# Optimization experiments

Hardware: AMD Instinct MI355X
Metric: run time of the kernel (lower is better)

## Reference

```python
import jax, jax.numpy as jnp
import numpy as np

SEQLEN = np.array([1024, 768, 512, 1536, 256, 1280, 512, 1024], dtype=np.int32)
HIDDEN = 2048
HEAD_NUM = 16


def setup_inputs() -> dict:
    key = jax.random.key(0)
    k1, k2 = jax.random.split(key)
    total = int(SEQLEN.sum())
    a = jax.random.normal(k1, (total, HIDDEN), dtype=jnp.float32) * 0.02
    b = jax.random.normal(k2, (total, HIDDEN), dtype=jnp.float32) * 0.02
    return {"a": a, "b": b, "seqlen": np.asarray(SEQLEN), "head_num": HEAD_NUM}


def reference(a, b, seqlen, head_num):
    # Variable-length strided batched matmul (QK^T), no padding.
    # a, b: [sum(seqlen), hidden]; output: flat concat of per-seq [head_num, s, s].
    seqlen = np.asarray(seqlen)
    offs = np.concatenate([[0], np.cumsum(seqlen)])  # static offsets
    hidden = a.shape[1]
    head_size = hidden // head_num
    outs = []
    for i, s in enumerate(seqlen.tolist()):
        ai = a[offs[i]:offs[i + 1]].reshape(s, head_num, head_size)
        bi = b[offs[i]:offs[i + 1]].reshape(s, head_num, head_size)
        # per-head QK^T: [head_num, s, s]
        ci = jnp.einsum('shd,thd->hst', ai, bi)
        outs.append(ci.reshape(-1))
    return jnp.concatenate(outs)
```

## Files before the change

kernel.cpp:

```cpp
#include <hip/hip_runtime.h>

#define NSEQ   8
#define HEADS  16
#define HSIZE  128
#define HIDDEN 2048
#define BT     128
#define LDS_PAD 8
#define LDS_ROW (HSIZE + LDS_PAD)

typedef __attribute__((ext_vector_type(8))) short  bf16x8;
typedef __attribute__((ext_vector_type(4))) float  f32x4;

struct SeqMap {
    int       s[NSEQ];
    int       row_off[NSEQ];
    long long out_off[NSEQ];
    int       t[NSEQ];
    int       blk_start[NSEQ];
    int       nblk;
};

__device__ __forceinline__ unsigned short f2bf(float x) {
    unsigned int u = __builtin_bit_cast(unsigned int, x);
    u += 0x7fffu + ((u >> 16) & 1u);
    return (unsigned short)(u >> 16);
}

__device__ __forceinline__ ushort4 f2bf4(float4 v) {
    ushort4 p;
    p.x = f2bf(v.x); p.y = f2bf(v.y); p.z = f2bf(v.z); p.w = f2bf(v.w);
    return p;
}

__global__ __launch_bounds__(256, 2) void qkt_pipe_kernel(
    const float* __restrict__ A, const float* __restrict__ B,
    float* __restrict__ out, SeqMap map)
{
    __shared__ unsigned short lds[2][BT * LDS_ROW];

    const int cpx = map.nblk >> 3;
    const int bid = ((int)blockIdx.x % 8) * cpx + ((int)blockIdx.x / 8);

    int i = 0;
    #pragma unroll
    for (int k = 1; k < NSEQ; ++k) if (bid >= map.blk_start[k]) i = k;
    const int local = bid - map.blk_start[i];
    const int t     = map.t[i];
    const int h     = local / t;
    const int tr    = local - h * t;
    const int s     = map.s[i];
    const int row0  = map.row_off[i];

    const int tid  = threadIdx.x;
    const int r0   = tid >> 5;
    const int c4   = tid & 31;
    const size_t hcol = (size_t)h * HSIZE + (size_t)c4 * 4;

    const int lane = tid & 63;
    const int w    = tid >> 6;
    const int wr   = w >> 1;
    const int wc   = w & 1;
    const int lrow = lane & 15;
    const int kgrp = lane >> 4;

    unsigned short* ldsw0 = &lds[0][r0 * LDS_ROW + c4 * 4];
    unsigned short* ldsw1 = &lds[1][r0 * LDS_ROW + c4 * 4];

    float4 g[16];

    {
        const float* sa = A + (size_t)(row0 + tr * BT + r0) * HIDDEN + hcol;
        #pragma unroll
        for (int it = 0; it < 16; ++it) g[it] = *(const float4*)(sa + (size_t)it * 8 * HIDDEN);
        #pragma unroll
        for (int it = 0; it < 16; ++it)
            *(ushort4*)(ldsw0 + it * 8 * LDS_ROW) = f2bf4(g[it]);
    }
    __syncthreads();

    bf16x8 af[4][4];
    #pragma unroll
    for (int m = 0; m < 4; ++m)
        #pragma unroll
        for (int kk = 0; kk < 4; ++kk)
            af[m][kk] = *(const bf16x8*)&lds[0][(wr*64 + m*16 + lrow) * LDS_ROW + kk*32 + kgrp*8];
    __syncthreads();

    {
        const float* sb = B + (size_t)(row0 + r0) * HIDDEN + hcol;
        #pragma unroll
        for (int it = 0; it < 16; ++it) g[it] = *(const float4*)(sb + (size_t)it * 8 * HIDDEN);
        #pragma unroll
        for (int it = 0; it < 16; ++it)
            *(ushort4*)(ldsw0 + it * 8 * LDS_ROW) = f2bf4(g[it]);
    }
    if (t > 1) {
        const float* sb = B + (size_t)(row0 + BT + r0) * HIDDEN + hcol;
        #pragma unroll
        for (int it = 0; it < 16; ++it) g[it] = *(const float4*)(sb + (size_t)it * 8 * HIDDEN);
    }
    __syncthreads();

    int cur = 0;
    const long long obase = map.out_off[i] + (long long)h * s * s;
    float* orow = out + obase
                + (long long)(tr * BT + wr * 64 + lrow) * s
                + (wc * 64 + kgrp * 4);
    const long long s16 = (long long)s * 16;

    const float* sbpre = B + (size_t)(row0 + 2 * BT + r0) * HIDDEN + hcol;

    for (int tc = 0; tc < t; ++tc) {
        if (tc + 1 < t) {
            unsigned short* dst = cur ? ldsw0 : ldsw1;
            #pragma unroll
            for (int it = 0; it < 16; ++it)
                *(ushort4*)(dst + it * 8 * LDS_ROW) = f2bf4(g[it]);
        }

        if (tc + 2 < t) {
            #pragma unroll
            for (int it = 0; it < 16; ++it) g[it] = *(const float4*)(sbpre + (size_t)it * 8 * HIDDEN);
            sbpre += (size_t)BT * HIDDEN;
        }

        f32x4 acc[4][4];
        #pragma unroll
        for (int m = 0; m < 4; ++m)
            #pragma unroll
            for (int n = 0; n < 4; ++n)
                acc[m][n] = (f32x4){0.f, 0.f, 0.f, 0.f};

        const unsigned short* lb = &lds[cur][0];
        #pragma unroll
        for (int kk = 0; kk < 4; ++kk) {
            bf16x8 bfr[4];
            #pragma unroll
            for (int n = 0; n < 4; ++n)
                bfr[n] = *(const bf16x8*)&lb[(wc*64 + n*16 + lrow) * LDS_ROW + kk*32 + kgrp*8];
            #pragma unroll
            for (int m = 0; m < 4; ++m)
                #pragma unroll
                for (int n = 0; n < 4; ++n)
                    acc[m][n] = __builtin_amdgcn_mfma_f32_16x16x32_bf16(
                                    bfr[n], af[m][kk], acc[m][n], 0, 0, 0);
        }

        {
            float* op = orow + tc * BT;
            #pragma unroll
            for (int m = 0; m < 4; ++m)
                #pragma unroll
                for (int n = 0; n < 4; ++n)
                    *(f32x4*)(op + (long long)m * s16 + n * 16) = acc[m][n];
        }

        if (tc + 1 < t) {
            asm volatile("s_waitcnt lgkmcnt(0)" ::: "memory");
            __builtin_amdgcn_s_barrier();
        }
        cur ^= 1;
    }
}

extern "C" void kernel_launch(void* const* d_in, const int* in_sizes, int n_in,
                              void* d_out, int out_size, void* d_ws, size_t ws_size,
                              hipStream_t stream) {
    const float* A = (const float*)d_in[0];
    const float* B = (const float*)d_in[1];
    float* out = (float*)d_out;

    static const int S[NSEQ] = {1024, 768, 512, 1536, 256, 1280, 512, 1024};

    int row_off[NSEQ]; long long out_off[NSEQ];
    int row = 0; long long o = 0;
    for (int i = 0; i < NSEQ; ++i) {
        row_off[i] = row; out_off[i] = o;
        row += S[i];
        o   += (long long)HEADS * S[i] * S[i];
    }

    static const int order[NSEQ] = {3, 5, 0, 7, 1, 2, 6, 4};

    SeqMap map;
    int blk = 0;
    for (int k = 0; k < NSEQ; ++k) {
        const int i = order[k];
        const int t = S[i] / BT;
        map.s[k]         = S[i];
        map.row_off[k]   = row_off[i];
        map.out_off[k]   = out_off[i];
        map.t[k]         = t;
        map.blk_start[k] = blk;
        blk += HEADS * t;
    }
    map.nblk = blk;

    qkt_pipe_kernel<<<blk, 256, 0, stream>>>(A, B, out, map);
}
```

Baseline: 211.0 us.

## Shrink B column tile to 64 and restructure the double-buffered pipeline

Each iteration now processes a 64-column B tile instead of 128, halving the LDS footprint and the per-thread register staging (8 float4 instead of 16) so that launch bounds can request 3 blocks per CU. The prefetch now loads only one tile ahead, and the bf16 conversion into LDS is moved after the MFMA block so global loads can overlap compute. The A tile is staged through both LDS buffers. The cost is twice as many iterations and barriers per block, and a full __syncthreads per step replaces the conditional lgkmcnt wait plus barrier.

```diff
diff --git a/kernel.cpp b/kernel.cpp
--- a/kernel.cpp
+++ b/kernel.cpp
@@ -4,7 +4,8 @@
 #define HEADS  16
 #define HSIZE  128
 #define HIDDEN 2048
-#define BT     128
+#define BM     128
+#define BN     64
 #define LDS_PAD 8
 #define LDS_ROW (HSIZE + LDS_PAD)
 
@@ -32,11 +33,11 @@
     return p;
 }
 
-__global__ __launch_bounds__(256, 2) void qkt_pipe_kernel(
+__global__ __launch_bounds__(256, 3) void qkt_strip64_kernel(
     const float* __restrict__ A, const float* __restrict__ B,
     float* __restrict__ out, SeqMap map)
 {
-    __shared__ unsigned short lds[2][BT * LDS_ROW];
+    __shared__ unsigned short lds[2][BN * LDS_ROW];
 
     const int cpx = map.nblk >> 3;
     const int bid = ((int)blockIdx.x % 8) * cpx + ((int)blockIdx.x / 8);
@@ -50,6 +51,7 @@
     const int tr    = local - h * t;
     const int s     = map.s[i];
     const int row0  = map.row_off[i];
+    const int t2    = t * 2;
 
     const int tid  = threadIdx.x;
     const int r0   = tid >> 5;
@@ -66,15 +68,19 @@
     unsigned short* ldsw0 = &lds[0][r0 * LDS_ROW + c4 * 4];
     unsigned short* ldsw1 = &lds[1][r0 * LDS_ROW + c4 * 4];
 
-    float4 g[16];
-
     {
-        const float* sa = A + (size_t)(row0 + tr * BT + r0) * HIDDEN + hcol;
-        #pragma unroll
-        for (int it = 0; it < 16; ++it) g[it] = *(const float4*)(sa + (size_t)it * 8 * HIDDEN);
-        #pragma unroll
-        for (int it = 0; it < 16; ++it)
-            *(ushort4*)(ldsw0 + it * 8 * LDS_ROW) = f2bf4(g[it]);
+        const float* sa = A + (size_t)(row0 + tr * BM + r0) * HIDDEN + hcol;
+        float4 ga[8], gb[8];
+        #pragma unroll
+        for (int it = 0; it < 8; ++it) ga[it] = *(const float4*)(sa + (size_t)it * 8 * HIDDEN);
+        #pragma unroll
+        for (int it = 0; it < 8; ++it) gb[it] = *(const float4*)(sa + (size_t)(64 + it * 8) * HIDDEN);
+        #pragma unroll
+        for (int it = 0; it < 8; ++it)
+            *(ushort4*)(ldsw0 + it * 8 * LDS_ROW) = f2bf4(ga[it]);
+        #pragma unroll
+        for (int it = 0; it < 8; ++it)
+            *(ushort4*)(ldsw1 + it * 8 * LDS_ROW) = f2bf4(gb[it]);
     }
     __syncthreads();
 
@@ -83,83 +89,78 @@
     for (int m = 0; m < 4; ++m)
         #pragma unroll
         for (int kk = 0; kk < 4; ++kk)
-            af[m][kk] = *(const bf16x8*)&lds[0][(wr*64 + m*16 + lrow) * LDS_ROW + kk*32 + kgrp*8];
+            af[m][kk] = *(const bf16x8*)&lds[wr][(m*16 + lrow) * LDS_ROW + kk*32 + kgrp*8];
     __syncthreads();
 
     {
         const float* sb = B + (size_t)(row0 + r0) * HIDDEN + hcol;
-        #pragma unroll
-        for (int it = 0; it < 16; ++it) g[it] = *(const float4*)(sb + (size_t)it * 8 * HIDDEN);
-        #pragma unroll
-        for (int it = 0; it < 16; ++it)
-            *(ushort4*)(ldsw0 + it * 8 * LDS_ROW) = f2bf4(g[it]);
-    }
-    if (t > 1) {
-        const float* sb = B + (size_t)(row0 + BT + r0) * HIDDEN + hcol;
-        #pragma unroll
-        for (int it = 0; it < 16; ++it) g[it] = *(const float4*)(sb + (size_t)it * 8 * HIDDEN);
+        float4 gb[8];
+        #pragma unroll
+        for (int it = 0; it < 8; ++it) gb[it] = *(const float4*)(sb + (size_t)it * 8 * HIDDEN);
+        #pragma unroll
+        for (int it = 0; it < 8; ++it)
+            *(ushort4*)(ldsw0 + it * 8 * LDS_ROW) = f2bf4(gb[it]);
     }
     __syncthreads();
 
-    int cur = 0;
     const long long obase = map.out_off[i] + (long long)h * s * s;
     float* orow = out + obase
-                + (long long)(tr * BT + wr * 64 + lrow) * s
-                + (wc * 64 + kgrp * 4);
+                + (long long)(tr * BM + wr * 64 + lrow) * s
+                + (wc * 32 + kgrp * 4);
     const long long s16 = (long long)s * 16;
 
-    const float* sbpre = B + (size_t)(row0 + 2 * BT + r0) * HIDDEN + hcol;
-
-    for (int tc = 0; tc < t; ++tc) {
-        if (tc + 1 < t) {
-            unsigned short* dst = cur ? ldsw0 : ldsw1;
-            #pragma unroll
-            for (int it = 0; it < 16; ++it)
-                *(ushort4*)(dst + it * 8 * LDS_ROW) = f2bf4(g[it]);
-        }
-
-        if (tc + 2 < t) {
-            #pragma unroll
-            for (int it = 0; it < 16; ++it) g[it] = *(const float4*)(sbpre + (size_t)it * 8 * HIDDEN);
-            sbpre += (size_t)BT * HIDDEN;
-        }
-
-        f32x4 acc[4][4];
+    const float* sbnext = B + (size_t)(row0 + BN + r0) * HIDDEN + hcol;
+
+    for (int tc = 0; tc < t2; ++tc) {
+        const bool has_next = (tc + 1 < t2);
+        const int  cur = tc & 1;
+
+        float4 g[8];
+        if (has_next) {
+            #pragma unroll
+            for (int it = 0; it < 8; ++it) g[it] = *(const float4*)(sbnext + (size_t)it * 8 * HIDDEN);
+            sbnext += (size_t)BN * HIDDEN;
+        }
+
+        f32x4 acc[4][2];
         #pragma unroll
         for (int m = 0; m < 4; ++m)
             #pragma unroll
-            for (int n = 0; n < 4; ++n)
+            for (int n = 0; n < 2; ++n)
                 acc[m][n] = (f32x4){0.f, 0.f, 0.f, 0.f};
 
         const unsigned short* lb = &lds[cur][0];
         #pragma unroll
         for (int kk = 0; kk < 4; ++kk) {
-            bf16x8 bfr[4];
-            #pragma unroll
-            for (int n = 0; n < 4; ++n)
-                bfr[n] = *(const bf16x8*)&lb[(wc*64 + n*16 + lrow) * LDS_ROW + kk*32 + kgrp*8];
+            bf16x8 bfr[2];
+            #pragma unroll
+            for (int n = 0; n < 2; ++n)
+                bfr[n] = *(const bf16x8*)&lb[(wc*32 + n*16 + lrow) * LDS_ROW + kk*32 + kgrp*8];
             #pragma unroll
             for (int m = 0; m < 4; ++m)
                 #pragma unroll
-                for (int n = 0; n < 4; ++n)
+                for (int n = 0; n < 2; ++n)
                     acc[m][n] = __builtin_amdgcn_mfma_f32_16x16x32_bf16(
                                     bfr[n], af[m][kk], acc[m][n], 0, 0, 0);
         }
 
+        if (has_next) {
+            unsigned short* dst = cur ? ldsw0 : ldsw1;
+            #pragma unroll
+            for (int it = 0; it < 8; ++it)
+                *(ushort4*)(dst + it * 8 * LDS_ROW) = f2bf4(g[it]);
+        }
+
         {
-            float* op = orow + tc * BT;
+            float* op = orow + tc * BN;
             #pragma unroll
             for (int m = 0; m < 4; ++m)
                 #pragma unroll
-                for (int n = 0; n < 4; ++n)
+                for (int n = 0; n < 2; ++n)
                     *(f32x4*)(op + (long long)m * s16 + n * 16) = acc[m][n];
         }
 
-        if (tc + 1 < t) {
-            asm volatile("s_waitcnt lgkmcnt(0)" ::: "memory");
-            __builtin_amdgcn_s_barrier();
-        }
-        cur ^= 1;
+        __syncthreads();
     }
 }
 
@@ -186,7 +187,7 @@
     int blk = 0;
     for (int k = 0; k < NSEQ; ++k) {
         const int i = order[k];
-        const int t = S[i] / BT;
+        const int t = S[i] / BM;
         map.s[k]         = S[i];
         map.row_off[k]   = row_off[i];
         map.out_off[k]   = out_off[i];
@@ -196,5 +197,5 @@
     }
     map.nblk = blk;
 
-    qkt_pipe_kernel<<<blk, 256, 0, stream>>>(A, B, out, map);
-}
+    qkt_strip64_kernel<<<blk, 256, 0, stream>>>(A, B, out, map);
+}
```

Result: slower. 295.8 us (+40.2%).
